# Optimization experiments

Hardware: AMD Instinct MI355X
Metric: run time of the kernel (lower is better)

The kernel has to match this reference:

```python
import jax, jax.numpy as jnp
import numpy as np

B, D, H, O, C, L = 16384, 1024, 1024, 256, 8, 3  # batch, input, hidden, output, num_classes, num_layers


def setup_inputs() -> dict:
    key = jax.random.key(0)
    ks = jax.random.split(key, 9)
    s_in = 1.0 / np.sqrt(D)
    s_h = 1.0 / np.sqrt(H)
    return {
        "x": jax.random.normal(ks[0], (B, D), jnp.float32),
        # classifier: Linear(D, C)
        "Wc": jax.random.normal(ks[1], (D, C), jnp.float32) * s_in,
        "bc": jnp.zeros((C,), jnp.float32),
        # per-branch first linear: Linear(D, H), stacked over C branches
        "W1": jax.random.normal(ks[2], (C, D, H), jnp.float32) * s_in,
        "b1": jnp.zeros((C, H), jnp.float32),
        # per-branch hidden linears: (num_layers-1) x Linear(H, H)
        "W2": jax.random.normal(ks[3], (C, L - 1, H, H), jnp.float32) * s_h,
        "b2": jnp.zeros((C, L - 1, H), jnp.float32),
        # per-branch output linear: Linear(H, O)
        "Wo": jax.random.normal(ks[4], (C, H, O), jnp.float32) * s_h,
        "bo": jnp.zeros((C, O), jnp.float32),
    }


def reference(x, Wc, bc, W1, b1, W2, b2, Wo, bo):
    # classifier logits: (B, C)
    logits = x @ Wc + bc
    # argmax routing (no target_bin given), clamped as in torch
    class_idx = jnp.clip(jnp.argmax(logits, axis=-1), 0, C - 1)
    one_hot = jax.nn.one_hot(class_idx, C, dtype=x.dtype)  # (B, C)
    # dense compute-all-branches, faithful to the torch module
    h = jax.nn.relu(jnp.einsum("bd,cdh->bch", x, W1) + b1)  # (B, C, H)
    for i in range(L - 1):
        h = jax.nn.relu(jnp.einsum("bch,chk->bck", h, W2[:, i]) + b2[:, i])
    outputs = jnp.einsum("bch,cho->bco", h, Wo) + bo  # (B, C, O)
    output = jnp.sum(one_hot[:, :, None] * outputs, axis=1)  # (B, O)
    return output, logits
```

## Files before the change

### kernel.cpp

```cpp
#include <hip/hip_runtime.h>
#include <stdint.h>

#define BB 16384
#define DD 1024
#define HH 1024
#define OO 256
#define CC 8

typedef unsigned short u16;
typedef __attribute__((ext_vector_type(4))) unsigned short u16x4;
typedef __attribute__((ext_vector_type(8))) short bf16x8;
typedef __attribute__((ext_vector_type(4))) float f32x4;

__device__ __forceinline__ u16 f2bf(float f) {
    union { float f; uint32_t u; } v; v.f = f;
    const uint32_t u = v.u;
    return (u16)((u + 0x7FFFu + ((u >> 16) & 1u)) >> 16);
}

#define GLDS16(g, l)                                                                   \
    __builtin_amdgcn_global_load_lds((const __attribute__((address_space(1))) void*)(g), \
                                     (__attribute__((address_space(3))) void*)(l), 16, 0, 0)

__global__ __launch_bounds__(256)
void transpose_bf16_kernel(const float* __restrict__ src, u16* __restrict__ dst,
                           int R, int Cc)
{
    __shared__ float t[32][33];
    const int tid = threadIdx.x;
    const int mat = blockIdx.z;
    const int r0 = blockIdx.y * 32, c0 = blockIdx.x * 32;
    {
        const int rr = tid >> 3, c4 = (tid & 7) * 4;
        const float4 v = *(const float4*)(src + ((size_t)mat * R + r0 + rr) * Cc + c0 + c4);
        t[rr][c4 + 0] = v.x; t[rr][c4 + 1] = v.y; t[rr][c4 + 2] = v.z; t[rr][c4 + 3] = v.w;
    }
    __syncthreads();
    {
        const int cc = tid >> 3, k4 = (tid & 7) * 4;
        u16x4 o;
        o[0] = f2bf(t[k4 + 0][cc]);
        o[1] = f2bf(t[k4 + 1][cc]);
        o[2] = f2bf(t[k4 + 2][cc]);
        o[3] = f2bf(t[k4 + 3][cc]);
        *(u16x4*)(dst + ((size_t)mat * Cc + c0 + cc) * R + r0 + k4) = o;
    }
}

__global__ __launch_bounds__(256)
void logits_kernel(const float* __restrict__ x, const float* __restrict__ Wc,
                   const float* __restrict__ bc, float* __restrict__ logits_out,
                   u16* __restrict__ x_bf16, int* __restrict__ class_idx,
                   int* __restrict__ hist)
{
    __shared__ float WcT[CC][DD];
    __shared__ int clsarr[16];
    const int tid = threadIdx.x;
    #pragma unroll
    for (int j = 0; j < 8; ++j) {
        const int f = tid + 256 * j;
        const float4 v = ((const float4*)Wc)[f];
        const int d = f >> 1, c = (f & 1) * 4;
        WcT[c + 0][d] = v.x; WcT[c + 1][d] = v.y; WcT[c + 2][d] = v.z; WcT[c + 3][d] = v.w;
    }
    __syncthreads();

    const int lane = tid & 63, wv = tid >> 6;
    const int row0 = blockIdx.x * 16 + wv * 4;

    float acc[4][8];
    #pragma unroll
    for (int r = 0; r < 4; ++r)
        #pragma unroll
        for (int c = 0; c < 8; ++c) acc[r][c] = 0.f;

    #pragma unroll
    for (int p = 0; p < 2; ++p) {
        float4 xv[2][4];
        #pragma unroll
        for (int rr = 0; rr < 2; ++rr) {
            const float4* xr = (const float4*)(x + (size_t)(row0 + 2 * p + rr) * DD);
            #pragma unroll
            for (int j = 0; j < 4; ++j) xv[rr][j] = xr[lane + 64 * j];
        }
        #pragma unroll
        for (int rr = 0; rr < 2; ++rr) {
            u16* xb = x_bf16 + (size_t)(row0 + 2 * p + rr) * DD;
            #pragma unroll
            for (int j = 0; j < 4; ++j) {
                const float4 v = xv[rr][j];
                u16x4 o; o[0] = f2bf(v.x); o[1] = f2bf(v.y); o[2] = f2bf(v.z); o[3] = f2bf(v.w);
                *(u16x4*)(xb + 4 * (lane + 64 * j)) = o;
            }
        }
        #pragma unroll
        for (int j = 0; j < 4; ++j) {
            const int f = lane + 64 * j;
            #pragma unroll
            for (int c = 0; c < 8; ++c) {
                const float4 w = *(const float4*)&WcT[c][4 * f];
                #pragma unroll
                for (int rr = 0; rr < 2; ++rr)
                    acc[2 * p + rr][c] += xv[rr][j].x * w.x + xv[rr][j].y * w.y
                                        + xv[rr][j].z * w.z + xv[rr][j].w * w.w;
            }
        }
    }

    #pragma unroll
    for (int off = 8; off < 64; off <<= 1)
        #pragma unroll
        for (int r = 0; r < 4; ++r)
            #pragma unroll
            for (int c = 0; c < 8; ++c)
                acc[r][c] += __shfl_xor(acc[r][c], off, 64);

    const int cls = lane >> 3;
    const float bcv = bc[cls];
    float s[4];
    #pragma unroll
    for (int r = 0; r < 4; ++r) {
        float v = acc[r][0];
        #pragma unroll
        for (int c = 1; c < 8; ++c) v = (cls == c) ? acc[r][c] : v;
        s[r] = v;
    }
    #pragma unroll
    for (int off = 1; off < 8; off <<= 1)
        #pragma unroll
        for (int r = 0; r < 4; ++r) s[r] += __shfl_xor(s[r], off, 64);
    #pragma unroll
    for (int r = 0; r < 4; ++r) s[r] += bcv;

    #pragma unroll
    for (int r = 0; r < 4; ++r)
        if ((lane & 7) == 0) logits_out[(size_t)(row0 + r) * CC + cls] = s[r];

    int idx[4] = {cls, cls, cls, cls};
    #pragma unroll
    for (int off = 8; off < 64; off <<= 1) {
        #pragma unroll
        for (int r = 0; r < 4; ++r) {
            const float ov = __shfl_xor(s[r], off, 64);
            const int oi = __shfl_xor(idx[r], off, 64);
            const bool take = (ov > s[r]) || (ov == s[r] && oi < idx[r]);
            s[r] = take ? ov : s[r];
            idx[r] = take ? oi : idx[r];
        }
    }
    if (lane == 0) {
        #pragma unroll
        for (int r = 0; r < 4; ++r) {
            class_idx[row0 + r] = idx[r];
            clsarr[wv * 4 + r] = idx[r];
        }
    }
    __syncthreads();
    if (tid < 64) {
        const int myc = (tid < 16) ? clsarr[tid] : -1;
        int h = 0;
        #pragma unroll
        for (int cc = 0; cc < 8; ++cc) {
            const int p = __popcll(__ballot(myc == cc));
            h = (tid == cc) ? p : h;
        }
        if (tid < 8) hist[blockIdx.x * 8 + tid] = h;
    }
}

__global__ __launch_bounds__(256)
void scan_kernel(const int* __restrict__ hist, int* __restrict__ offsets,
                 int* __restrict__ bb)
{
    const int t = threadIdx.x, c = t >> 5, g = t & 31;
    int sum = 0;
    #pragma unroll 4
    for (int i = 0; i < 32; ++i) sum += hist[(g * 32 + i) * 8 + c];
    int inc = sum;
    #pragma unroll
    for (int d = 1; d < 32; d <<= 1) {
        const int v = __shfl_up(inc, d, 32);
        if (g >= d) inc += v;
    }
    __shared__ int tot[8], offL[9];
    if (g == 31) tot[c] = inc;
    __syncthreads();
    if (t == 0) {
        int o = 0; offL[0] = 0; offsets[0] = 0;
        #pragma unroll
        for (int c8 = 0; c8 < 8; ++c8) {
            o += (tot[c8] + 127) & ~127;
            offL[c8 + 1] = o; offsets[c8 + 1] = o;
        }
    }
    __syncthreads();
    int base = offL[c] + (inc - sum);
    #pragma unroll 4
    for (int i = 0; i < 32; ++i) {
        const int b = g * 32 + i;
        bb[b * 8 + c] = base;
        base += hist[b * 8 + c];
    }
}

__global__ __launch_bounds__(256)
void scatter_kernel(const int* __restrict__ class_idx, const int* __restrict__ bb,
                    int* __restrict__ rowidx)
{
    const int r = blockIdx.x * 256 + threadIdx.x;
    const int c = class_idx[r];
    const int lane = threadIdx.x & 63;
    const int gl = lane & ~15;
    const unsigned long long before = (1ull << lane) - (1ull << gl);
    int rank = 0;
    #pragma unroll
    for (int cc = 0; cc < 8; ++cc) {
        const unsigned long long m = __ballot(c == cc);
        const int p = __popcll(m & before);
        rank = (c == cc) ? p : rank;
    }
    rowidx[bb[(r >> 4) * 8 + c] + rank] = r;
}

#define MF(a, b, c) __builtin_amdgcn_mfma_f32_16x16x32_bf16((a), (b), (c), 0, 0, 0)

template<bool GATHER_A>
__global__ __launch_bounds__(256)
void gemm_kernel(const u16* __restrict__ Abase, const u16* __restrict__ Wbase,
                 size_t wclass_stride, const float* __restrict__ bias_base,
                 int bias_stride, const int* __restrict__ offsets,
                 const int* __restrict__ rowidx, u16* __restrict__ Hout)
{
    __shared__ u16 sA[2 * 8192];
    __shared__ u16 sB[2 * 8192];
    const int tid = threadIdx.x;

    const int bid = blockIdx.x;
    const int wg = (bid & 7) * ((int)gridDim.x >> 3) + (bid >> 3);
    const int m0 = (wg >> 3) * 128;
    const int n0 = (wg & 7) * 128;
    if (m0 >= offsets[CC]) return;
    int c = 0;
    while (m0 >= offsets[c + 1]) ++c;

    const u16* const Wcl = Wbase + (size_t)c * wclass_stride;

    const u16* gsA[4]; const u16* gsB[4];
    int dn[4];
    #pragma unroll
    for (int j = 0; j < 4; ++j) {
        const int n = tid + 256 * j;
        const int row = n >> 3;
        const int logc = (n & 7) ^ (row & 7);
        int grow = m0 + row;
        if (GATHER_A) { const int g = rowidx[grow]; grow = (g < 0) ? 0 : g; }
        gsA[j] = Abase + (size_t)grow * 1024 + logc * 8;
        gsB[j] = Wcl + (size_t)(n0 + row) * 1024 + logc * 8;
        dn[j] = n * 8;
    }

#define STAGE(SB, KT)                                                     \
    { GLDS16(gsA[0] + (KT) * 64, sA + (SB) * 8192 + dn[0]);               \
      GLDS16(gsA[1] + (KT) * 64, sA + (SB) * 8192 + dn[1]);               \
      GLDS16(gsA[2] + (KT) * 64, sA + (SB) * 8192 + dn[2]);               \
      GLDS16(gsA[3] + (KT) * 64, sA + (SB) * 8192 + dn[3]);               \
      GLDS16(gsB[0] + (KT) * 64, sB + (SB) * 8192 + dn[0]);               \
      GLDS16(gsB[1] + (KT) * 64, sB + (SB) * 8192 + dn[1]);               \
      GLDS16(gsB[2] + (KT) * 64, sB + (SB) * 8192 + dn[2]);               \
      GLDS16(gsB[3] + (KT) * 64, sB + (SB) * 8192 + dn[3]); }

    const int wv = tid >> 6, ln = tid & 63;
    const int wm = (wv & 1) * 64, wn = (wv >> 1) * 64;
    const int lr = ln & 15, lg = ln >> 4;
    const int s7 = lr & 7;
    const int pc0 = ((0 * 4 + lg) ^ s7) * 8;
    const int pc1 = ((1 * 4 + lg) ^ s7) * 8;
    const u16* const fA = sA + (wm + lr) * 64;
    const u16* const fB = sB + (wn + lr) * 64;

    f32x4 acc[4][4];
    #pragma unroll
    for (int i = 0; i < 4; ++i)
        #pragma unroll
        for (int j = 0; j < 4; ++j)
            acc[i][j] = (f32x4){0.f, 0.f, 0.f, 0.f};

#define COMPUTE(SB)                                                       \
    {                                                                     \
        bf16x8 a0[4], b0[4], a1[4], b1[4];                                \
        _Pragma("unroll")                                                 \
        for (int i = 0; i < 4; ++i) {                                     \
            a0[i] = *(const bf16x8*)(fA + (SB) * 8192 + i * 1024 + pc0);  \
            b0[i] = *(const bf16x8*)(fB + (SB) * 8192 + i * 1024 + pc0);  \
        }                                                                 \
        __builtin_amdgcn_s_setprio(1);                                    \
        _Pragma("unroll")                                                 \
        for (int mi = 0; mi < 4; ++mi)                                    \
            _Pragma("unroll")                                             \
            for (int ni = 0; ni < 4; ++ni)                                \
                acc[mi][ni] = MF(a0[mi], b0[ni], acc[mi][ni]);            \
        __builtin_amdgcn_s_setprio(0);                                    \
        _Pragma("unroll")                                                 \
        for (int i = 0; i < 4; ++i) {                                     \
            a1[i] = *(const bf16x8*)(fA + (SB) * 8192 + i * 1024 + pc1);  \
            b1[i] = *(const bf16x8*)(fB + (SB) * 8192 + i * 1024 + pc1);  \
        }                                                                 \
        __builtin_amdgcn_s_setprio(1);                                    \
        _Pragma("unroll")                                                 \
        for (int mi = 0; mi < 4; ++mi)                                    \
            _Pragma("unroll")                                             \
            for (int ni = 0; ni < 4; ++ni)                                \
                acc[mi][ni] = MF(a1[mi], b1[ni], acc[mi][ni]);            \
        __builtin_amdgcn_s_setprio(0);                                    \
    }

    STAGE(0, 0);
    __syncthreads();
    for (int t = 0; t < 14; t += 2) {
        STAGE(1, t + 1); COMPUTE(0); __syncthreads();
        STAGE(0, t + 2); COMPUTE(1); __syncthreads();
    }
    STAGE(1, 15); COMPUTE(0); __syncthreads();
    COMPUTE(1);

#undef COMPUTE
#undef STAGE

    const float* bp = bias_base + (size_t)c * bias_stride + n0 + wn + lr;
    #pragma unroll
    for (int ni = 0; ni < 4; ++ni) {
        const float bv = bp[ni * 16];
        const int col = n0 + wn + ni * 16 + lr;
        #pragma unroll
        for (int mi = 0; mi < 4; ++mi) {
            const int rb = m0 + wm + mi * 16 + lg * 4;
            #pragma unroll
            for (int q = 0; q < 4; ++q) {
                float v = acc[mi][ni][q] + bv;
                v = v > 0.f ? v : 0.f;
                Hout[(size_t)(rb + q) * HH + col] = f2bf(v);
            }
        }
    }
}

#define STAGE4(b, kt)                           \
    {                                           \
        const int kb_ = (kt) * 32;              \
        GLDS16(gA0 + kb_, lA0 + (b) * 4096);    \
        GLDS16(gA1 + kb_, lA1 + (b) * 4096);    \
        GLDS16(gB0 + kb_, lB0 + (b) * 4096);    \
        GLDS16(gB1 + kb_, lB1 + (b) * 4096);    \
    }

#define COMPUTE4(b)                                                       \
    {                                                                     \
        bf16x8 af[4], bfr[4];                                             \
        _Pragma("unroll")                                                 \
        for (int i = 0; i < 4; ++i) {                                     \
            af[i]  = *(const bf16x8*)(fA + (b) * 4096 + i * 16 * 32);     \
            bfr[i] = *(const bf16x8*)(fB + (b) * 4096 + i * 16 * 32);     \
        }                                                                 \
        __builtin_amdgcn_s_setprio(1);                                    \
        _Pragma("unroll")                                                 \
        for (int mi = 0; mi < 4; ++mi)                                    \
            _Pragma("unroll")                                             \
            for (int ni = 0; ni < 4; ++ni)                                \
                acc[mi][ni] = __builtin_amdgcn_mfma_f32_16x16x32_bf16(    \
                    af[mi], bfr[ni], acc[mi][ni], 0, 0, 0);               \
        __builtin_amdgcn_s_setprio(0);                                    \
    }

#define WAITV(N)                                                          \
    asm volatile("s_waitcnt vmcnt(" #N ")" ::: "memory");                 \
    __builtin_amdgcn_s_barrier();                                         \
    __builtin_amdgcn_sched_barrier(0);

__global__ __launch_bounds__(256, 3)
void gemm_final_kernel(const u16* __restrict__ Abase, const u16* __restrict__ Wbase,
                       size_t wclass_stride, const float* __restrict__ bias_base,
                       int bias_stride, const int* __restrict__ offsets,
                       const int* __restrict__ rowidx, float* __restrict__ Fout)
{
    __shared__ u16 sA[3 * 128 * 32];
    __shared__ u16 sB[3 * 128 * 32];
    const int tid = threadIdx.x;

    const int bid = blockIdx.x;
    const int wg = (bid & 7) * ((int)gridDim.x >> 3) + (bid >> 3);
    const int m0 = (wg >> 1) * 128;
    const int n0 = (wg & 1) * 128;
    if (m0 >= offsets[CC]) return;
    int c = 0;
    while (m0 >= offsets[c + 1]) ++c;

    const int srow = tid >> 2;
    const int kc8 = (tid & 3) * 8;
    const int sa0 = m0 + srow, sa1 = m0 + srow + 64;
    const u16* gA0 = Abase + (size_t)sa0 * 1024 + kc8;
    const u16* gA1 = Abase + (size_t)sa1 * 1024 + kc8;
    const u16* Wcl = Wbase + (size_t)c * wclass_stride;
    const u16* gB0 = Wcl + (size_t)(n0 + srow) * 1024 + kc8;
    const u16* gB1 = Wcl + (size_t)(n0 + srow + 64) * 1024 + kc8;
    u16* lA0 = sA + tid * 8;
    u16* lA1 = sA + 2048 + tid * 8;
    u16* lB0 = sB + tid * 8;
    u16* lB1 = sB + 2048 + tid * 8;

    const int lane = tid & 63, wv = tid >> 6;
    const int wm = (wv & 1) * 64, wn = (wv >> 1) * 64;
    const int lr = lane & 15, lg = lane >> 4;
    const u16* fA = sA + (wm + lr) * 32 + lg * 8;
    const u16* fB = sB + (wn + lr) * 32 + lg * 8;

    f32x4 acc[4][4];
    #pragma unroll
    for (int i = 0; i < 4; ++i)
        #pragma unroll
        for (int j = 0; j < 4; ++j)
            acc[i][j] = (f32x4){0.f, 0.f, 0.f, 0.f};

    STAGE4(0, 0);
    STAGE4(1, 1);
    for (int kt = 0; kt < 30; kt += 3) {
        WAITV(4);
        STAGE4(2, kt + 2);
        COMPUTE4(0);
        WAITV(4);
        STAGE4(0, kt + 3);
        COMPUTE4(1);
        WAITV(4);
        STAGE4(1, kt + 4);
        COMPUTE4(2);
    }
    WAITV(4);
    COMPUTE4(0);
    WAITV(0);
    COMPUTE4(1);

    const float* bp = bias_base + (size_t)c * bias_stride + n0 + wn + lr;
    #pragma unroll
    for (int ni = 0; ni < 4; ++ni) {
        const float bv = bp[ni * 16];
        const int col = n0 + wn + ni * 16 + lr;
        #pragma unroll
        for (int mi = 0; mi < 4; ++mi) {
            const int rb = m0 + wm + mi * 16 + lg * 4;
            #pragma unroll
            for (int q = 0; q < 4; ++q) {
                const float v = acc[mi][ni][q] + bv;
                const int orow = rowidx[rb + q];
                if (orow >= 0) Fout[(size_t)orow * OO + col] = v;
            }
        }
    }
}

extern "C" void kernel_launch(void* const* d_in, const int* in_sizes, int n_in,
                              void* d_out, int out_size, void* d_ws, size_t ws_size,
                              hipStream_t stream)
{
    const float* x  = (const float*)d_in[0];
    const float* Wc = (const float*)d_in[1];
    const float* bc = (const float*)d_in[2];
    const float* W1 = (const float*)d_in[3];
    const float* b1 = (const float*)d_in[4];
    const float* W2 = (const float*)d_in[5];
    const float* b2 = (const float*)d_in[6];
    const float* Wo = (const float*)d_in[7];
    const float* bo = (const float*)d_in[8];
    float* out    = (float*)d_out;
    float* logits = out + (size_t)BB * OO;

    char* ws = (char*)d_ws;
    constexpr size_t PADMAX = BB + CC * 128;
    constexpr int NLB = BB / 16;
    int* offsets   = (int*)(ws + 0);
    int* hist      = (int*)(ws + 64);
    int* bb        = (int*)(ws + 64 + NLB * 32);
    int* class_idx = (int*)(ws + 64 + 2 * NLB * 32);
    int* rowidx    = (int*)((char*)class_idx + (size_t)BB * 4);
    u16* x_bf16    = (u16*)((char*)rowidx + PADMAX * 4);
    u16* hA  = x_bf16 + (size_t)BB * DD;
    u16* hB  = hA + PADMAX * HH;
    u16* W1T = hB + PADMAX * HH;
    u16* W2T = W1T + (size_t)CC * DD * HH;
    u16* WoT = W2T + (size_t)CC * 2 * HH * HH;

    hipMemsetAsync(rowidx, 0xFF, PADMAX * 4, stream);

    transpose_bf16_kernel<<<dim3(32, 32, 8),  256, 0, stream>>>(W1, W1T, DD, HH);
    transpose_bf16_kernel<<<dim3(32, 32, 16), 256, 0, stream>>>(W2, W2T, HH, HH);
    transpose_bf16_kernel<<<dim3(8, 32, 8),   256, 0, stream>>>(Wo, WoT, HH, OO);

    logits_kernel<<<NLB, 256, 0, stream>>>(x, Wc, bc, logits, x_bf16, class_idx, hist);
    scan_kernel<<<1, 256, 0, stream>>>(hist, offsets, bb);
    scatter_kernel<<<BB / 256, 256, 0, stream>>>(class_idx, bb, rowidx);

    constexpr int MT = (int)(PADMAX / 128);
    gemm_kernel<true ><<<dim3(MT * 8), 256, 0, stream>>>(
        x_bf16, W1T, (size_t)DD * HH, b1, HH, offsets, rowidx, hA);
    gemm_kernel<false><<<dim3(MT * 8), 256, 0, stream>>>(
        hA, W2T, (size_t)2 * HH * HH, b2, 2 * HH, offsets, rowidx, hB);
    gemm_kernel<false><<<dim3(MT * 8), 256, 0, stream>>>(
        hB, W2T + (size_t)HH * HH, (size_t)2 * HH * HH, b2 + HH, 2 * HH, offsets, rowidx, hA);
    gemm_final_kernel<<<dim3(MT * 2), 256, 0, stream>>>(
        hA, WoT, (size_t)OO * HH, bo, OO, offsets, rowidx, out);
}
```

Before: 320.2 us.

## Enlarge hidden GEMM M-tile to 256 with K-step 32 and 256-row class padding

```diff
diff --git a/kernel.cpp b/kernel.cpp
--- a/kernel.cpp
+++ b/kernel.cpp
@@ -189,7 +189,7 @@
         int o = 0; offL[0] = 0; offsets[0] = 0;
         #pragma unroll
         for (int c8 = 0; c8 < 8; ++c8) {
-            o += (tot[c8] + 127) & ~127;
+            o += (tot[c8] + 255) & ~255;
             offL[c8 + 1] = o; offsets[c8 + 1] = o;
         }
     }
@@ -223,6 +223,8 @@
 }
 
 #define MF(a, b, c) __builtin_amdgcn_mfma_f32_16x16x32_bf16((a), (b), (c), 0, 0, 0)
+#define ASZ 8192
+#define BSZ 4096
 
 template<bool GATHER_A>
 __global__ __launch_bounds__(256)
@@ -231,13 +233,13 @@
                  int bias_stride, const int* __restrict__ offsets,
                  const int* __restrict__ rowidx, u16* __restrict__ Hout)
 {
-    __shared__ u16 sA[2 * 8192];
-    __shared__ u16 sB[2 * 8192];
+    __shared__ u16 sA[2 * ASZ];
+    __shared__ u16 sB[2 * BSZ];
     const int tid = threadIdx.x;
 
     const int bid = blockIdx.x;
     const int wg = (bid & 7) * ((int)gridDim.x >> 3) + (bid >> 3);
-    const int m0 = (wg >> 3) * 128;
+    const int m0 = (wg >> 3) * 256;
     const int n0 = (wg & 7) * 128;
     if (m0 >= offsets[CC]) return;
     int c = 0;
@@ -245,95 +247,87 @@
 
     const u16* const Wcl = Wbase + (size_t)c * wclass_stride;
 
-    const u16* gsA[4]; const u16* gsB[4];
-    int dn[4];
-    #pragma unroll
-    for (int j = 0; j < 4; ++j) {
-        const int n = tid + 256 * j;
-        const int row = n >> 3;
-        const int logc = (n & 7) ^ (row & 7);
-        int grow = m0 + row;
-        if (GATHER_A) { const int g = rowidx[grow]; grow = (g < 0) ? 0 : g; }
-        gsA[j] = Abase + (size_t)grow * 1024 + logc * 8;
-        gsB[j] = Wcl + (size_t)(n0 + row) * 1024 + logc * 8;
-        dn[j] = n * 8;
+    const u16* gsrc[6];
+    int dn[6];
+    #pragma unroll
+    for (int j = 0; j < 6; ++j) {
+        if (j < 4) {
+            const int n = tid + 256 * j;
+            const int row = n >> 2;
+            const int logc = (n & 3) ^ ((row >> 1) & 3);
+            int grow = m0 + row;
+            if (GATHER_A) { const int g = rowidx[grow]; grow = (g < 0) ? 0 : g; }
+            gsrc[j] = Abase + (size_t)grow * 1024 + logc * 8;
+            dn[j] = n * 8;
+        } else {
+            const int n = tid + 256 * (j - 4);
+            const int row = n >> 2;
+            const int logc = (n & 3) ^ ((row >> 1) & 3);
+            gsrc[j] = Wcl + (size_t)(n0 + row) * 1024 + logc * 8;
+            dn[j] = n * 8;
+        }
     }
 
 #define STAGE(SB, KT)                                                     \
-    { GLDS16(gsA[0] + (KT) * 64, sA + (SB) * 8192 + dn[0]);               \
-      GLDS16(gsA[1] + (KT) * 64, sA + (SB) * 8192 + dn[1]);               \
-      GLDS16(gsA[2] + (KT) * 64, sA + (SB) * 8192 + dn[2]);               \
-      GLDS16(gsA[3] + (KT) * 64, sA + (SB) * 8192 + dn[3]);               \
-      GLDS16(gsB[0] + (KT) * 64, sB + (SB) * 8192 + dn[0]);               \
-      GLDS16(gsB[1] + (KT) * 64, sB + (SB) * 8192 + dn[1]);               \
-      GLDS16(gsB[2] + (KT) * 64, sB + (SB) * 8192 + dn[2]);               \
-      GLDS16(gsB[3] + (KT) * 64, sB + (SB) * 8192 + dn[3]); }
+    { GLDS16(gsrc[0] + (KT) * 32, sA + (SB) * ASZ + dn[0]);               \
+      GLDS16(gsrc[1] + (KT) * 32, sA + (SB) * ASZ + dn[1]);               \
+      GLDS16(gsrc[2] + (KT) * 32, sA + (SB) * ASZ + dn[2]);               \
+      GLDS16(gsrc[3] + (KT) * 32, sA + (SB) * ASZ + dn[3]);               \
+      GLDS16(gsrc[4] + (KT) * 32, sB + (SB) * BSZ + dn[4]);               \
+      GLDS16(gsrc[5] + (KT) * 32, sB + (SB) * BSZ + dn[5]); }
 
     const int wv = tid >> 6, ln = tid & 63;
-    const int wm = (wv & 1) * 64, wn = (wv >> 1) * 64;
+    const int wm = wv >> 1, wn = wv & 1;
     const int lr = ln & 15, lg = ln >> 4;
-    const int s7 = lr & 7;
-    const int pc0 = ((0 * 4 + lg) ^ s7) * 8;
-    const int pc1 = ((1 * 4 + lg) ^ s7) * 8;
-    const u16* const fA = sA + (wm + lr) * 64;
-    const u16* const fB = sB + (wn + lr) * 64;
-
-    f32x4 acc[4][4];
-    #pragma unroll
-    for (int i = 0; i < 4; ++i)
+    const int pc = (lg ^ ((lr >> 1) & 3)) * 8;
+    const u16* const fA = sA + (wm * 128 + lr) * 32 + pc;
+    const u16* const fB = sB + (wn * 64 + lr) * 32 + pc;
+
+    f32x4 acc[8][4];
+    #pragma unroll
+    for (int i = 0; i < 8; ++i)
         #pragma unroll
         for (int j = 0; j < 4; ++j)
             acc[i][j] = (f32x4){0.f, 0.f, 0.f, 0.f};
 
 #define COMPUTE(SB)                                                       \
     {                                                                     \
-        bf16x8 a0[4], b0[4], a1[4], b1[4];                                \
+        bf16x8 bfr[4];                                                    \
         _Pragma("unroll")                                                 \
-        for (int i = 0; i < 4; ++i) {                                     \
-            a0[i] = *(const bf16x8*)(fA + (SB) * 8192 + i * 1024 + pc0);  \
-            b0[i] = *(const bf16x8*)(fB + (SB) * 8192 + i * 1024 + pc0);  \
-        }                                                                 \
+        for (int ni = 0; ni < 4; ++ni)                                    \
+            bfr[ni] = *(const bf16x8*)(fB + (SB) * BSZ + ni * 512);       \
         __builtin_amdgcn_s_setprio(1);                                    \
         _Pragma("unroll")                                                 \
-        for (int mi = 0; mi < 4; ++mi)                                    \
-            _Pragma("unroll")                                             \
-            for (int ni = 0; ni < 4; ++ni)                                \
-                acc[mi][ni] = MF(a0[mi], b0[ni], acc[mi][ni]);            \
-        __builtin_amdgcn_s_setprio(0);                                    \
-        _Pragma("unroll")                                                 \
-        for (int i = 0; i < 4; ++i) {                                     \
-            a1[i] = *(const bf16x8*)(fA + (SB) * 8192 + i * 1024 + pc1);  \
-            b1[i] = *(const bf16x8*)(fB + (SB) * 8192 + i * 1024 + pc1);  \
+        for (int mi = 0; mi < 8; ++mi) {                                  \
+            const bf16x8 a = *(const bf16x8*)(fA + (SB) * ASZ + mi * 512);\
+            acc[mi][0] = MF(a, bfr[0], acc[mi][0]);                       \
+            acc[mi][1] = MF(a, bfr[1], acc[mi][1]);                       \
+            acc[mi][2] = MF(a, bfr[2], acc[mi][2]);                       \
+            acc[mi][3] = MF(a, bfr[3], acc[mi][3]);                       \
         }                                                                 \
-        __builtin_amdgcn_s_setprio(1);                                    \
-        _Pragma("unroll")                                                 \
-        for (int mi = 0; mi < 4; ++mi)                                    \
-            _Pragma("unroll")                                             \
-            for (int ni = 0; ni < 4; ++ni)                                \
-                acc[mi][ni] = MF(a1[mi], b1[ni], acc[mi][ni]);            \
         __builtin_amdgcn_s_setprio(0);                                    \
     }
 
     STAGE(0, 0);
     __syncthreads();
-    for (int t = 0; t < 14; t += 2) {
+    for (int t = 0; t < 30; t += 2) {
         STAGE(1, t + 1); COMPUTE(0); __syncthreads();
         STAGE(0, t + 2); COMPUTE(1); __syncthreads();
     }
-    STAGE(1, 15); COMPUTE(0); __syncthreads();
+    STAGE(1, 31); COMPUTE(0); __syncthreads();
     COMPUTE(1);
 
 #undef COMPUTE
 #undef STAGE
 
-    const float* bp = bias_base + (size_t)c * bias_stride + n0 + wn + lr;
+    const float* bp = bias_base + (size_t)c * bias_stride + n0 + wn * 64 + lr;
     #pragma unroll
     for (int ni = 0; ni < 4; ++ni) {
         const float bv = bp[ni * 16];
-        const int col = n0 + wn + ni * 16 + lr;
-        #pragma unroll
-        for (int mi = 0; mi < 4; ++mi) {
-            const int rb = m0 + wm + mi * 16 + lg * 4;
+        const int col = n0 + wn * 64 + ni * 16 + lr;
+        #pragma unroll
+        for (int mi = 0; mi < 8; ++mi) {
+            const int rb = m0 + wm * 128 + mi * 16 + lg * 4;
             #pragma unroll
             for (int q = 0; q < 4; ++q) {
                 float v = acc[mi][ni][q] + bv;
@@ -473,7 +467,7 @@
     float* logits = out + (size_t)BB * OO;
 
     char* ws = (char*)d_ws;
-    constexpr size_t PADMAX = BB + CC * 128;
+    constexpr size_t PADMAX = BB + CC * 256;
     constexpr int NLB = BB / 16;
     int* offsets   = (int*)(ws + 0);
     int* hist      = (int*)(ws + 64);
@@ -497,13 +491,14 @@
     scan_kernel<<<1, 256, 0, stream>>>(hist, offsets, bb);
     scatter_kernel<<<BB / 256, 256, 0, stream>>>(class_idx, bb, rowidx);
 
-    constexpr int MT = (int)(PADMAX / 128);
-    gemm_kernel<true ><<<dim3(MT * 8), 256, 0, stream>>>(
+    constexpr int MT2 = (int)(PADMAX / 256);
+    constexpr int MT4 = (int)(PADMAX / 128);
+    gemm_kernel<true ><<<dim3(MT2 * 8), 256, 0, stream>>>(
         x_bf16, W1T, (size_t)DD * HH, b1, HH, offsets, rowidx, hA);
-    gemm_kernel<false><<<dim3(MT * 8), 256, 0, stream>>>(
+    gemm_kernel<false><<<dim3(MT2 * 8), 256, 0, stream>>>(
         hA, W2T, (size_t)2 * HH * HH, b2, 2 * HH, offsets, rowidx, hB);
-    gemm_kernel<false><<<dim3(MT * 8), 256, 0, stream>>>(
+    gemm_kernel<false><<<dim3(MT2 * 8), 256, 0, stream>>>(
         hB, W2T + (size_t)HH * HH, (size_t)2 * HH * HH, b2 + HH, 2 * HH, offsets, rowidx, hA);
-    gemm_final_kernel<<<dim3(MT * 2), 256, 0, stream>>>(
+    gemm_final_kernel<<<dim3(MT4 * 2), 256, 0, stream>>>(
         hA, WoT, (size_t)OO * HH, bo, OO, offsets, rowidx, out);
 }
```

Measured after the change: 419.3 us. 30.9% more time.
